# Kernel tuning notes

Measured on AMD Instinct MI355X. Metric: run time of the kernel, lower is better.

## Reference

```python
import jax, jax.numpy as jnp
import numpy as np

NBINS = 30
LO, HI = -6.0, 6.0
BINWIDTH = (HI - LO) / (NBINS - 2)  # interior bin width, matches abs((hi-lo)/(nbins-2))


def setup_inputs() -> dict:
    key = jax.random.key(0)
    x = jax.random.normal(key, (4096, 16384), dtype=jnp.float32)
    return {"x": x}


def reference(x):
    # Single-pass digitize + scatter-add, mathematically identical to the
    # original per-bin threshold-compare loop:
    #   bin 0 (orig BinPop[1]):      x <  LO
    #   bin i (orig BinPop[i+1]):    LO+(i-1)*w <= x < LO+i*w, i=1..nbins-2
    #   bin nbins-1 (BinPop[nbins]): x >= HI   (HI == LO + (nbins-2)*w)
    b, n = x.shape
    k = jnp.clip(jnp.floor((x - LO) / BINWIDTH), -1.0, NBINS - 2).astype(jnp.int32) + 1
    rows = jnp.arange(b, dtype=jnp.int32)[:, None]  # [b,1] broadcast against [b,n]
    hist_nat = jnp.zeros((b, NBINS), dtype=x.dtype).at[rows, k].add(1.0)
    # The original concatenates dict values in insertion order:
    # [bin1, bin_nbins, bin2, ..., bin_{nbins-1}]
    order = np.concatenate([[0], [NBINS - 1], np.arange(1, NBINS - 1)])
    return hist_nat[:, order]
```

## Files before the change

### kernel.cpp

```cpp
#include <hip/hip_runtime.h>


#define NBINS   30
#define THREADS 256
#define ROWLEN  16384
#define ITERS   (ROWLEN / 4 / THREADS)

typedef float f4 __attribute__((ext_vector_type(4)));

__global__ __launch_bounds__(THREADS, 4) void hist_kernel(
    const float* __restrict__ x, float* __restrict__ out)
{
    __shared__ unsigned int h[NBINS * THREADS];
    __shared__ unsigned int partial[8 * NBINS];

    const int t   = threadIdx.x;
    const int row = blockIdx.x;

#pragma unroll
    for (int b = 0; b < NBINS; ++b) h[b * THREADS + t] = 0u;
    __syncthreads();

    const float W    = (float)(12.0 / 28.0);
    const float invW = 1.0f / W;
    const float c6   = 6.0f * invW;

    const f4* xr = (const f4*)(x + (size_t)row * ROWLEN);
    const int base = THREADS + t;

#pragma unroll
    for (int i = 0; i < ITERS; ++i) {
        f4 v = __builtin_nontemporal_load(&xr[t + i * THREADS]);
        {
            int k = __float2int_rd(fmaf(v.x, invW, c6));
            k = min(max(k, -1), NBINS - 2);
            atomicAdd(&h[k * THREADS + base], 1u);
        }
        {
            int k = __float2int_rd(fmaf(v.y, invW, c6));
            k = min(max(k, -1), NBINS - 2);
            atomicAdd(&h[k * THREADS + base], 1u);
        }
        {
            int k = __float2int_rd(fmaf(v.z, invW, c6));
            k = min(max(k, -1), NBINS - 2);
            atomicAdd(&h[k * THREADS + base], 1u);
        }
        {
            int k = __float2int_rd(fmaf(v.w, invW, c6));
            k = min(max(k, -1), NBINS - 2);
            atomicAdd(&h[k * THREADS + base], 1u);
        }
    }
    __syncthreads();

    if (t < 240) {
        const int b = t % NBINS;
        const int g = t / NBINS;
        unsigned int s = 0;
#pragma unroll
        for (int i = 0; i < 32; ++i)
            s += h[b * THREADS + g * 32 + ((i + b) & 31)];
        partial[g * NBINS + b] = s;
    }
    __syncthreads();

    if (t < NBINS) {
        unsigned int s = 0;
#pragma unroll
        for (int g = 0; g < 8; ++g) s += partial[g * NBINS + t];
        const int dst = (t == 0) ? 0 : (t == NBINS - 1) ? 1 : (t + 1);
        out[(size_t)row * NBINS + dst] = (float)s;
    }
}

extern "C" void kernel_launch(void* const* d_in, const int* in_sizes, int n_in,
                              void* d_out, int out_size, void* d_ws, size_t ws_size,
                              hipStream_t stream)
{
    const float* x  = (const float*)d_in[0];
    float* out      = (float*)d_out;
    const int rows  = in_sizes[0] / ROWLEN;
    hist_kernel<<<rows, THREADS, 0, stream>>>(x, out);
}
```

Measured before the change: 334.6 us.

## Software-pipeline row loads with register double buffering and clamp bins in float

```diff
diff --git a/kernel.cpp b/kernel.cpp
--- a/kernel.cpp
+++ b/kernel.cpp
@@ -4,11 +4,12 @@
 #define NBINS   30
 #define THREADS 256
 #define ROWLEN  16384
-#define ITERS   (ROWLEN / 4 / THREADS)
+#define VPG     4
+#define GROUPS  (ROWLEN / 4 / THREADS / VPG)
 
 typedef float f4 __attribute__((ext_vector_type(4)));
 
-__global__ __launch_bounds__(THREADS, 4) void hist_kernel(
+__global__ __launch_bounds__(THREADS) void hist_kernel(
     const float* __restrict__ x, float* __restrict__ out)
 {
     __shared__ unsigned int h[NBINS * THREADS];
@@ -21,36 +22,37 @@
     for (int b = 0; b < NBINS; ++b) h[b * THREADS + t] = 0u;
     __syncthreads();
 
-    const float W    = (float)(12.0 / 28.0);
-    const float invW = 1.0f / W;
-    const float c6   = 6.0f * invW;
+    const float invW = 28.0f / 12.0f;
+    const float c15  = 15.0f;
 
     const f4* xr = (const f4*)(x + (size_t)row * ROWLEN);
-    const int base = THREADS + t;
 
+    f4 cur[VPG], nxt[VPG];
 #pragma unroll
-    for (int i = 0; i < ITERS; ++i) {
-        f4 v = __builtin_nontemporal_load(&xr[t + i * THREADS]);
-        {
-            int k = __float2int_rd(fmaf(v.x, invW, c6));
-            k = min(max(k, -1), NBINS - 2);
-            atomicAdd(&h[k * THREADS + base], 1u);
+    for (int j = 0; j < VPG; ++j)
+        cur[j] = __builtin_nontemporal_load(&xr[t + j * THREADS]);
+
+#pragma unroll 1
+    for (int g = 0; g < GROUPS; ++g) {
+        if (g + 1 < GROUPS) {
+#pragma unroll
+            for (int j = 0; j < VPG; ++j)
+                nxt[j] = __builtin_nontemporal_load(
+                    &xr[t + ((g + 1) * VPG + j) * THREADS]);
         }
-        {
-            int k = __float2int_rd(fmaf(v.y, invW, c6));
-            k = min(max(k, -1), NBINS - 2);
-            atomicAdd(&h[k * THREADS + base], 1u);
+#pragma unroll
+        for (int j = 0; j < VPG; ++j) {
+            f4 v = cur[j];
+#pragma unroll
+            for (int c = 0; c < 4; ++c) {
+                float f = fmaf(v[c], invW, c15);
+                f = fminf(fmaxf(f, 0.0f), 29.0f);
+                int bin = __float2int_rd(f);
+                atomicAdd(&h[bin * THREADS + t], 1u);
+            }
         }
-        {
-            int k = __float2int_rd(fmaf(v.z, invW, c6));
-            k = min(max(k, -1), NBINS - 2);
-            atomicAdd(&h[k * THREADS + base], 1u);
-        }
-        {
-            int k = __float2int_rd(fmaf(v.w, invW, c6));
-            k = min(max(k, -1), NBINS - 2);
-            atomicAdd(&h[k * THREADS + base], 1u);
-        }
+#pragma unroll
+        for (int j = 0; j < VPG; ++j) cur[j] = nxt[j];
     }
     __syncthreads();
 
```

Measured after the change: 327.3 us. 1.02x faster.
